# Kernel tuning notes

Hardware: AMD Instinct MI355X
Metric: run time of the kernel (lower is better)

## Reference

```python
import jax, jax.numpy as jnp
import numpy as np

PRIOR_VAR = 0.01
NUM_HEADS = 12
EMBED_DIM = 768


def kl_regularizer(mu, logvar):
    kl_loss = (jnp.log(PRIOR_VAR) - 1.0 - logvar
               + jax.nn.softplus(logvar) / PRIOR_VAR
               + jnp.square(mu) / PRIOR_VAR)
    return 0.5 * jnp.mean(kl_loss)


def linear_vdp(mu_in, Sigma_in, w_mu, w_sigma):
    # mu_in, Sigma_in: [..., Din]; w_mu: [Din, Dout]; w_sigma: [Dout]
    mu_out = mu_in @ w_mu
    kl = kl_regularizer(w_mu, w_sigma)
    W_Sigma = jax.nn.softplus(w_sigma)                      # [Dout]
    din = w_mu.shape[0]
    # w_t_Sigma_i_w: w scaled by sqrt(Din)
    w_scaled = w_mu / jnp.sqrt(jnp.float32(din))
    Sigma_1 = Sigma_in @ (w_scaled * w_scaled)              # [..., Dout]
    # x_Sigma_w_x_T: x scaled by Din
    x = mu_in / jnp.float32(din)
    xx_t = jnp.sum(x * x, axis=-1, keepdims=True)
    Sigma_2 = xx_t * W_Sigma
    # tr_Sigma_w_Sigma_in
    Sigma_3 = jnp.sum(Sigma_in, axis=-1, keepdims=True) * W_Sigma / jnp.float32(w_mu.shape[-1])
    Sigma_out = jax.nn.softplus(Sigma_1 + Sigma_2 + Sigma_3)
    return mu_out, Sigma_out, kl


def split_heads(x, B, H, d):
    # [B, S, E] -> [B, H, S, d]
    return x.reshape(B, -1, H, d).transpose(0, 2, 1, 3)


def vdp_attention(mu_q, sg_q, mu_k, sg_k, mu_v, sg_v):
    d = jnp.float32(mu_k.shape[-1])
    sq = jnp.sqrt(d)
    mu_score = jnp.einsum('bhqd,bhkd->bhqk', mu_q, mu_k)
    a = jnp.einsum('bhqd,bhkd->bhqk', mu_q * mu_q / d, sg_k)
    b = jnp.einsum('bhid,bhjd->bhij', mu_k * mu_k / d, sg_q)  # TF matmul(key.., query.., transpose_b)
    c = jnp.einsum('bhqd,bhkd->bhqk', sg_q / sq, sg_k / sq)
    sigma_score = a + b + c
    mu_weights = jax.nn.softmax(mu_score / sq, axis=-1)
    wdim = jnp.float32(mu_weights.shape[-1])
    grad = jnp.square(mu_weights - mu_weights * mu_weights)
    Sigma_weights = grad * (sigma_score / d) / wdim
    mu_out = jnp.einsum('bhqk,bhkd->bhqd', mu_weights, mu_v)
    dterm = jnp.einsum('bhqk,bhkd->bhqd', mu_weights * mu_weights / wdim, sg_v)
    eterm = jnp.einsum('bhqk,bhkd->bhqd', Sigma_weights, mu_v * mu_v / wdim)
    fterm = jnp.einsum('bhqk,bhkd->bhqd', Sigma_weights / jnp.sqrt(wdim), sg_v / jnp.sqrt(wdim))
    out_sigma = jax.nn.softplus(dterm + eterm + fterm)
    return mu_out, out_sigma


def forward(mu_inputs, sigma_inputs, wq_mu, wq_sigma, wk_mu, wk_sigma,
            wv_mu, wv_sigma, wo_mu, wo_sigma):
    B = mu_inputs.shape[0]
    H = NUM_HEADS
    d = EMBED_DIM // H
    # VDP_Dropout with Training=False is identity
    mu_q, sg_q, kl_q = linear_vdp(mu_inputs, sigma_inputs, wq_mu, wq_sigma)
    mu_k, sg_k, kl_k = linear_vdp(mu_inputs, sigma_inputs, wk_mu, wk_sigma)
    mu_v, sg_v, kl_v = linear_vdp(mu_inputs, sigma_inputs, wv_mu, wv_sigma)
    mu_q, sg_q = split_heads(mu_q, B, H, d), split_heads(sg_q, B, H, d)
    mu_k, sg_k = split_heads(mu_k, B, H, d), split_heads(sg_k, B, H, d)
    mu_v, sg_v = split_heads(mu_v, B, H, d), split_heads(sg_v, B, H, d)
    mu_att, sg_att = vdp_attention(mu_q, sg_q, mu_k, sg_k, mu_v, sg_v)
    mu_cat = mu_att.transpose(0, 2, 1, 3).reshape(B, -1, EMBED_DIM)
    sg_cat = sg_att.transpose(0, 2, 1, 3).reshape(B, -1, EMBED_DIM)
    mu_out, Sigma_out, kl_c = linear_vdp(mu_cat, sg_cat, wo_mu, wo_sigma)
    Sigma_out = jax.nn.softplus(Sigma_out)
    kl = kl_q + kl_k + kl_v + kl_c
    return mu_out, Sigma_out, kl


def setup_inputs() -> dict:
    key = jax.random.key(0)
    ks = jax.random.split(key, 12)
    B, S, E = 4, 1024, EMBED_DIM
    glorot_std = np.sqrt(2.0 / (E + E)).astype(np.float32)
    def wsig(k):
        return jax.random.uniform(k, (E,), jnp.float32, -4.6, -2.25)
    return {
        'mu_inputs': jax.random.normal(ks[0], (B, S, E), jnp.float32),
        'sigma_inputs': jax.random.uniform(ks[1], (B, S, E), jnp.float32),
        'wq_mu': jax.random.normal(ks[2], (E, E), jnp.float32) * glorot_std,
        'wq_sigma': wsig(ks[3]),
        'wk_mu': jax.random.normal(ks[4], (E, E), jnp.float32) * glorot_std,
        'wk_sigma': wsig(ks[5]),
        'wv_mu': jax.random.normal(ks[6], (E, E), jnp.float32) * glorot_std,
        'wv_sigma': wsig(ks[7]),
        'wo_mu': jax.random.normal(ks[8], (E, E), jnp.float32) * glorot_std,
        'wo_sigma': wsig(ks[9]),
    }


def reference(mu_inputs, sigma_inputs, wq_mu, wq_sigma, wk_mu, wk_sigma,
              wv_mu, wv_sigma, wo_mu, wo_sigma):
    return forward(mu_inputs, sigma_inputs, wq_mu, wq_sigma, wk_mu, wk_sigma,
                   wv_mu, wv_sigma, wo_mu, wo_sigma)
```

## Files before the change

### kernel.cpp

```cpp
#include <hip/hip_runtime.h>
#include <math.h>

#define E 768
#define NTOK 4096

typedef __attribute__((ext_vector_type(8))) __bf16 bf16x8;
typedef __attribute__((ext_vector_type(4))) float f32x4;
typedef unsigned int u32;
typedef unsigned short u16;
typedef __attribute__((ext_vector_type(4))) u32 u32x4;

#define BFN ((size_t)NTOK * E)
#define WFN ((size_t)E * E)
#define QSC 1.4901161193847656e-08f
#define C2E 0.18033688011112042f

__device__ __forceinline__ float sp_f(float x) {
    return fmaxf(x, 0.f) + log1pf(__expf(-fabsf(x)));
}
__device__ __forceinline__ u16 f2bf(float f) {
    u32 u = __float_as_uint(f);
    u += 0x7fffu + ((u >> 16) & 1u);
    return (u16)(u >> 16);
}
__device__ __forceinline__ u32 pk2(float a, float b) {
    return (u32)f2bf(a) | ((u32)f2bf(b) << 16);
}
__device__ __forceinline__ u32 cvtpk(float a, float b) {
    u32 r; asm("v_cvt_pk_bf16_f32 %0, %1, %2" : "=v"(r) : "v"(a), "v"(b)); return r;
}
__device__ __forceinline__ float ex2(float x) {
    float r; asm("v_exp_f32 %0, %1" : "=v"(r) : "v"(x)); return r;
}
__device__ __forceinline__ float lg2(float x) {
    float r; asm("v_log_f32 %0, %1" : "=v"(r) : "v"(x)); return r;
}
__device__ __forceinline__ float bfl(u32 u) { return __uint_as_float(u << 16); }
__device__ __forceinline__ float bfh(u32 u) { return __uint_as_float(u & 0xffff0000u); }

#define GLL16(gp, lp) __builtin_amdgcn_global_load_lds( \
    (const __attribute__((address_space(1))) u32*)(gp), \
    (__attribute__((address_space(3))) u32*)(lp), 16, 0, 0)

#define SBAR() do { __builtin_amdgcn_sched_barrier(0); \
                    __builtin_amdgcn_s_barrier(); \
                    __builtin_amdgcn_sched_barrier(0); } while (0)
#define VMCNT(N) do { asm volatile("s_waitcnt vmcnt(" #N ")" ::: "memory"); \
                      __builtin_amdgcn_sched_barrier(0); } while (0)

__global__ __launch_bounds__(256) void prep_all(
    const float* __restrict__ mu_in, const float* __restrict__ sg_in,
    const float* __restrict__ wq, const float* __restrict__ wk,
    const float* __restrict__ wvp, const float* __restrict__ wo,
    const float* __restrict__ wqs, const float* __restrict__ wks,
    const float* __restrict__ wvs, const float* __restrict__ wos,
    u16* __restrict__ Xmu, u16* __restrict__ Xsg,
    float* __restrict__ rmu2, float* __restrict__ rsg,
    u16* __restrict__ WtAll, u16* __restrict__ W2tAll,
    float* __restrict__ spws, float* __restrict__ kl_out)
{
    __shared__ float T[32][33];
    __shared__ float r1[4], r2[4];
    const int b = blockIdx.x, tid = threadIdx.x;

    if (b < 2048) {
        const int half = tid >> 7;
        const int n = b * 2 + half;
        const int t2 = tid & 127;
        float s1 = 0.f, s2 = 0.f;
        if (t2 < 96) {
            size_t o = (size_t)n * E + t2 * 8;
            float4 a0 = *(const float4*)(mu_in + o), a1 = *(const float4*)(mu_in + o + 4);
            float4 b0 = *(const float4*)(sg_in + o), b1 = *(const float4*)(sg_in + o + 4);
            *(uint4*)(Xmu + o) = make_uint4(pk2(a0.x, a0.y), pk2(a0.z, a0.w), pk2(a1.x, a1.y), pk2(a1.z, a1.w));
            *(uint4*)(Xsg + o) = make_uint4(pk2(b0.x, b0.y), pk2(b0.z, b0.w), pk2(b1.x, b1.y), pk2(b1.z, b1.w));
            s1 = a0.x*a0.x + a0.y*a0.y + a0.z*a0.z + a0.w*a0.w + a1.x*a1.x + a1.y*a1.y + a1.z*a1.z + a1.w*a1.w;
            s2 = b0.x + b0.y + b0.z + b0.w + b1.x + b1.y + b1.z + b1.w;
        }
        for (int off = 32; off; off >>= 1) {
            s1 += __shfl_xor(s1, off);
            s2 += __shfl_xor(s2, off);
        }
        if ((tid & 63) == 0) { r1[tid >> 6] = s1; r2[tid >> 6] = s2; }
        __syncthreads();
        if (t2 == 0) {
            rmu2[n] = r1[half * 2] + r1[half * 2 + 1];
            rsg[n]  = r2[half * 2] + r2[half * 2 + 1];
        }
    } else if (b < 4352) {
        const int b2 = b - 2048;
        const int z = b2 / 576, rem = b2 - z * 576;
        const float* W = (z == 0) ? wq : (z == 1) ? wk : (z == 2) ? wvp : wo;
        u16* Wt  = WtAll  + (size_t)z * WFN;
        u16* W2t = W2tAll + (size_t)z * WFN;
        const int j0 = (rem % 24) * 32, k0 = (rem / 24) * 32;
        const int r = tid >> 3, c = (tid & 7) * 4;
        float4 v = *(const float4*)(W + (size_t)(k0 + r) * E + j0 + c);
        T[r][c] = v.x; T[r][c + 1] = v.y; T[r][c + 2] = v.z; T[r][c + 3] = v.w;
        __syncthreads();
        const int j = tid >> 3, kc = (tid & 7) * 4;
        float w0 = T[kc][j], w1 = T[kc + 1][j], w2 = T[kc + 2][j], w3 = T[kc + 3][j];
        size_t o = (size_t)(j0 + j) * E + k0 + kc;
        *(uint2*)(Wt + o) = make_uint2(pk2(w0, w1), pk2(w2, w3));
        const float s = 1.f / 768.f;
        *(uint2*)(W2t + o) = make_uint2(pk2(w0 * w0 * s, w1 * w1 * s), pk2(w2 * w2 * s, w3 * w3 * s));
    } else if (b < 4864) {
        const int gid = (b - 4352) * 256 + tid;
        const int gsz = 512 * 256;
        float acc = 0.f;
        const float cw = 100.f / ((float)E * (float)E);
#pragma unroll
        for (int mm = 0; mm < 4; ++mm) {
            const float* w  = (mm == 0) ? wq  : (mm == 1) ? wk  : (mm == 2) ? wvp : wo;
            const float* sv = (mm == 0) ? wqs : (mm == 1) ? wks : (mm == 2) ? wvs : wos;
            for (int i = gid; i < E * E; i += gsz) { float x = w[i]; acc += x * x * cw; }
            for (int i = gid; i < E; i += gsz) { float x = sv[i]; acc += (-x + sp_f(x) * 100.f) * (1.f / (float)E); }
        }
        if (b == 4352 && tid == 0) acc += 4.f * (logf(0.01f) - 1.f);
        for (int off = 32; off; off >>= 1) acc += __shfl_xor(acc, off);
        if ((tid & 63) == 0) r1[tid >> 6] = acc;
        __syncthreads();
        if (tid == 0) atomicAdd(kl_out, 0.5f * (r1[0] + r1[1] + r1[2] + r1[3]));
    } else {
        for (int i = tid; i < 4 * E; i += 256) {
            const float* src;
            int j;
            if (i < E)            { src = wqs; j = i; }
            else if (i < 2 * E)   { src = wks; j = i - E; }
            else if (i < 3 * E)   { src = wvs; j = i - 2 * E; }
            else                  { src = wos; j = i - 3 * E; }
            spws[i] = sp_f(src[j]);
        }
    }
}

template<int MODE, int NBUF>
__global__ __launch_bounds__(256, 3) void linear_fused(
    const u16* __restrict__ Am, const u16* __restrict__ As,
    const u16* __restrict__ Wt, const u16* __restrict__ W2t,
    const float* __restrict__ spws, const float* __restrict__ rmu2, const float* __restrict__ rsg,
    float* __restrict__ mu_out, float* __restrict__ sg_out, u16* __restrict__ QKVB)
{
    __shared__ __align__(16) u16 L[NBUF * 12288];

    const int wgid = blockIdx.x;
    const int xcd = wgid & 7, local = wgid >> 3;
    const int m_blk = xcd * 4 + (local & 3);
    const int n_blk = local >> 2;
    const int m0 = m_blk * 128, col0 = n_blk * 64;
    const int tid = threadIdx.x, wv = tid >> 6, lane = tid & 63;
    const int g = lane >> 4, q15 = lane & 15;

    const u16* sp_[6];
    {
        const int rA = tid >> 2, cA = tid & 3;
        const int rB = 64 + rA;
        const int csA = (cA ^ ((rA >> 1) & 3)) << 3;
        const int csB = (cA ^ ((rB >> 1) & 3)) << 3;
        sp_[0] = Am  + (size_t)(m0 + rA) * E + csA;
        sp_[1] = Am  + (size_t)(m0 + rB) * E + csB;
        sp_[2] = As  + (size_t)(m0 + rA) * E + csA;
        sp_[3] = As  + (size_t)(m0 + rB) * E + csB;
        sp_[4] = Wt  + (size_t)(col0 + rA) * E + csA;
        sp_[5] = W2t + (size_t)(col0 + rA) * E + csA;
    }

    f32x4 acc1[2][4], acc2[2][4];
#pragma unroll
    for (int mt = 0; mt < 2; ++mt)
#pragma unroll
        for (int nt = 0; nt < 4; ++nt) {
            acc1[mt][nt] = (f32x4){0.f, 0.f, 0.f, 0.f};
            acc2[mt][nt] = (f32x4){0.f, 0.f, 0.f, 0.f};
        }

#pragma unroll
    for (int j = 0; j < 6; ++j)
        GLL16(sp_[j], &L[j * 2048 + tid * 8]);

    for (int t = 0; t < 24; ++t) {
        SBAR();
        const int tn = (t < 23) ? t + 1 : 23;
        const int nb = ((t & 1) ^ 1) * 12288;
#pragma unroll
        for (int j = 0; j < 6; ++j)
            GLL16(sp_[j] + tn * 32, &L[nb + j * 2048 + tid * 8]);
        VMCNT(6);
        SBAR();
        const int cb = (t & 1) * 12288;
        bf16x8 am[2], asg[2];
#pragma unroll
        for (int mt = 0; mt < 2; ++mt) {
            int r = wv * 32 + mt * 16 + q15;
            int c = (g ^ ((r >> 1) & 3)) << 3;
            am[mt]  = *(const bf16x8*)&L[cb + r * 32 + c];
            asg[mt] = *(const bf16x8*)&L[cb + 4096 + r * 32 + c];
        }
        __builtin_amdgcn_s_setprio(1);
#pragma unroll
        for (int nt = 0; nt < 4; ++nt) {
            int rb = nt * 16 + q15;
            int c = (g ^ ((rb >> 1) & 3)) << 3;
            bf16x8 bw = *(const bf16x8*)&L[cb + 8192 + rb * 32 + c];
            bf16x8 b2 = *(const bf16x8*)&L[cb + 10240 + rb * 32 + c];
            acc1[0][nt] = __builtin_amdgcn_mfma_f32_16x16x32_bf16(am[0], bw, acc1[0][nt], 0, 0, 0);
            acc1[1][nt] = __builtin_amdgcn_mfma_f32_16x16x32_bf16(am[1], bw, acc1[1][nt], 0, 0, 0);
            acc2[0][nt] = __builtin_amdgcn_mfma_f32_16x16x32_bf16(asg[0], b2, acc2[0][nt], 0, 0, 0);
            acc2[1][nt] = __builtin_amdgcn_mfma_f32_16x16x32_bf16(asg[1], b2, acc2[1][nt], 0, 0, 0);
        }
        __builtin_amdgcn_s_setprio(0);
    }
    __syncthreads();

    const float inv2 = 1.f / (768.f * 768.f), invd = 1.f / 768.f;
    float rr[2][4];
#pragma unroll
    for (int mt = 0; mt < 2; ++mt)
#pragma unroll
        for (int r = 0; r < 4; ++r) {
            int row = m0 + wv * 32 + mt * 16 + g * 4 + r;
            rr[mt][r] = rmu2[row] * inv2 + rsg[row] * invd;
        }

    if (MODE == 0) {
#pragma unroll
        for (int mt = 0; mt < 2; ++mt)
#pragma unroll
            for (int nt = 0; nt < 4; ++nt)
#pragma unroll
                for (int r = 0; r < 4; ++r) {
                    int row = m0 + wv * 32 + mt * 16 + g * 4 + r;
                    int col = col0 + nt * 16 + q15;
                    float mu = acc1[mt][nt][r];
                    float sg = sp_f(sp_f(acc2[mt][nt][r] + rr[mt][r] * spws[col]));
                    mu_out[(size_t)row * E + col] = mu;
                    sg_out[(size_t)row * E + col] = sg;
                }
    } else {
        const int proj = n_blk / 12, h = n_blk % 12;
        float sgv[2][4][4];
#pragma unroll
        for (int mt = 0; mt < 2; ++mt)
#pragma unroll
            for (int nt = 0; nt < 4; ++nt)
#pragma unroll
                for (int r = 0; r < 4; ++r) {
                    int col = col0 + nt * 16 + q15;
                    sgv[mt][nt][r] = sp_f(acc2[mt][nt][r] + rr[mt][r] * spws[col]);
                }
        const int bb = m0 >> 10;
        if (proj < 2) {
            const int s0 = (m0 & 1023);
            const int sl = tid >> 1, hh = tid & 1;
            size_t gbase = ((size_t)(bb * 12 + h) << 16) + ((size_t)(s0 + sl) << 6) + hh * 32;
#pragma unroll
            for (int a = 0; a < 3; ++a) {
                __syncthreads();
#pragma unroll
                for (int mt = 0; mt < 2; ++mt)
#pragma unroll
                    for (int nt = 0; nt < 4; ++nt)
#pragma unroll
                        for (int r = 0; r < 4; ++r) {
                            float mu = acc1[mt][nt][r], sg = sgv[mt][nt][r];
                            float v = (a == 0) ? mu : (a == 1) ? sg :
                                      (proj == 0 ? (mu * mu + sg) * QSC : mu * mu * QSC);
                            L[(wv * 32 + mt * 16 + g * 4 + r) * 72 + nt * 16 + q15] = f2bf(v);
                        }
                __syncthreads();
                u16* dst = QKVB + (size_t)(proj * 3 + a) * BFN;
#pragma unroll
                for (int j = 0; j < 4; ++j)
                    *(uint4*)(dst + gbase + j * 8) = *(const uint4*)&L[sl * 72 + hh * 32 + j * 8];
            }
        } else {
            const int s0 = m0 & 1023;
#pragma unroll
            for (int a = 0; a < 3; ++a) {
                __syncthreads();
#pragma unroll
                for (int mt = 0; mt < 2; ++mt)
#pragma unroll
                    for (int nt = 0; nt < 4; ++nt)
#pragma unroll
                        for (int r = 0; r < 4; ++r) {
                            float mu = acc1[mt][nt][r], sg = sgv[mt][nt][r];
                            float v = (a == 0) ? mu : (a == 1) ? sg * 0.0009765625f : mu * mu + sg;
                            L[(nt * 16 + q15) * 136 + wv * 32 + g * 8 + mt * 4 + r] = f2bf(v);
                        }
                __syncthreads();
                const int d = tid >> 2, sc = (tid & 3) * 32;
                u16* dst = QKVB + (size_t)(6 + a) * BFN;
                size_t ga = ((size_t)((bb * 12 + h) * 64 + d) << 10) + s0 + sc;
                *(uint4*)(dst + ga)      = *(const uint4*)&L[d * 136 + sc];
                *(uint4*)(dst + ga + 8)  = *(const uint4*)&L[d * 136 + sc + 8];
                *(uint4*)(dst + ga + 16) = *(const uint4*)&L[d * 136 + sc + 16];
                *(uint4*)(dst + ga + 24) = *(const uint4*)&L[d * 136 + sc + 24];
            }
        }
    }
}

#define KB0 0
#define KB1 6144
#define VB0 12288
#define VB1 18432
__global__ __launch_bounds__(256, 3) void vdp_attn9(
    const u16* __restrict__ Kmu, const u16* __restrict__ Ksg, const u16* __restrict__ Asq,
    const u16* __restrict__ Qmu, const u16* __restrict__ Q1v, const u16* __restrict__ Q2v,
    const u16* __restrict__ Vmu, const u16* __restrict__ Vsg, const u16* __restrict__ Vw2,
    u16* __restrict__ om, u16* __restrict__ osg,
    float* __restrict__ armu2, float* __restrict__ arsg)
{
    __shared__ __align__(16) u16 L[24576];

    const int wgid = blockIdx.x;
    const int seq = (wgid & 7) * 96 + (wgid >> 3);
    const int bh = seq >> 4, qt = seq & 15;
    const int tid = threadIdx.x, wv = tid >> 6, lane = tid & 63;
    const int g = lane >> 4, q15 = lane & 15;
    const size_t hb = (size_t)bh << 16;

    const size_t qoff = hb + (size_t)((qt * 64 + wv * 16 + q15) << 6) + g * 8;
    bf16x8 bq0 = *(const bf16x8*)(Qmu + qoff), bq1 = *(const bf16x8*)(Qmu + qoff + 32);
    bf16x8 b10 = *(const bf16x8*)(Q1v + qoff), b11 = *(const bf16x8*)(Q1v + qoff + 32);
    bf16x8 b20 = *(const bf16x8*)(Q2v + qoff), b21 = *(const bf16x8*)(Q2v + qoff + 32);

    const int sr = tid >> 3, sc8 = tid & 7;
    const size_t koffA = hb + (size_t)sr * 64 + ((sc8 ^ (sr & 7)) << 3);
    const int vr = tid >> 2, vc = tid & 3;
    const size_t voff = hb + (size_t)vr * 1024 + ((vc ^ ((vr >> 1) & 3)) << 3);

    float m2 = -3.0e38f;
    float lacc[4] = {0.f, 0.f, 0.f, 0.f};
#pragma unroll
    for (int s = 0; s < 4; ++s)
        GLL16(Kmu + koffA + s * 2048, &L[s * 2048 + tid * 8]);
    __syncthreads();
    for (int t = 0; t < 8; ++t) {
        SBAR();
        const int tn = (t < 7) ? t + 1 : 7;
        const int nb = (t & 1) ? 0 : 8192;
#pragma unroll
        for (int s = 0; s < 4; ++s)
            GLL16(Kmu + koffA + (size_t)tn * 8192 + s * 2048, &L[nb + s * 2048 + tid * 8]);
        VMCNT(4);
        SBAR();
        const int kb = (t & 1) ? 8192 : 0;
        f32x4 sc[8];
#pragma unroll
        for (int kt = 0; kt < 8; ++kt) sc[kt] = (f32x4){0.f, 0.f, 0.f, 0.f};
        __builtin_amdgcn_s_setprio(1);
#pragma unroll
        for (int kt = 0; kt < 8; ++kt) {
            int row = kt * 16 + q15, ra = kb + (row << 6);
            bf16x8 k0 = *(const bf16x8*)&L[ra + ((g ^ (row & 7)) << 3)];
            bf16x8 k1 = *(const bf16x8*)&L[ra + (((g + 4) ^ (row & 7)) << 3)];
            sc[kt] = __builtin_amdgcn_mfma_f32_16x16x32_bf16(k0, bq0, sc[kt], 0, 0, 0);
            sc[kt] = __builtin_amdgcn_mfma_f32_16x16x32_bf16(k1, bq1, sc[kt], 0, 0, 0);
        }
        __builtin_amdgcn_s_setprio(0);
        float tmx = -3.0e38f;
#pragma unroll
        for (int kt = 0; kt < 8; ++kt)
#pragma unroll
            for (int r = 0; r < 4; ++r) tmx = fmaxf(tmx, sc[kt][r]);
        tmx *= C2E;
        if (tmx > m2 + 8.f) {
            float f = ex2(m2 - tmx);
            lacc[0] *= f; lacc[1] *= f; lacc[2] *= f; lacc[3] *= f;
            m2 = tmx;
        }
#pragma unroll
        for (int kt = 0; kt < 8; ++kt)
#pragma unroll
            for (int r = 0; r < 4; ++r)
                lacc[kt & 3] += ex2(fmaf(sc[kt][r], C2E, -m2));
    }
    __syncthreads();
    float l = (lacc[0] + lacc[1]) + (lacc[2] + lacc[3]);
#pragma unroll
    for (int off = 16; off <= 32; off <<= 1) {
        float mo = __shfl_xor(m2, off), lo = __shfl_xor(l, off);
        float nm = fmaxf(m2, mo);
        l = l * ex2(m2 - nm) + lo * ex2(mo - nm);
        m2 = nm;
    }
    const float M = m2 + lg2(l);

    f32x4 accm[4], accd[4], acce[4];
#pragma unroll
    for (int nt = 0; nt < 4; ++nt) {
        accm[nt] = (f32x4){0.f, 0.f, 0.f, 0.f};
        accd[nt] = (f32x4){0.f, 0.f, 0.f, 0.f};
        acce[nt] = (f32x4){0.f, 0.f, 0.f, 0.f};
    }

    GLL16(Kmu + koffA, &L[KB0 + 0    + wv * 512]);
    GLL16(Ksg + koffA, &L[KB0 + 2048 + wv * 512]);
    GLL16(Asq + koffA, &L[KB0 + 4096 + wv * 512]);
    GLL16(Vmu + voff, &L[VB0 + 0    + wv * 512]);
    GLL16(Vsg + voff, &L[VB0 + 2048 + wv * 512]);
    GLL16(Vw2 + voff, &L[VB0 + 4096 + wv * 512]);
    __syncthreads();

    for (int t = 0; t < 32; ++t) {
        SBAR();
        const int tn = (t < 31) ? t + 1 : 31;
        const size_t ka = (size_t)tn << 11;
        const size_t va = (size_t)tn << 5;
        const int nbK = (t & 1) ? KB0 : KB1;
        const int nbV = (t & 1) ? VB0 : VB1;
        GLL16(Kmu + koffA + ka, &L[nbK + 0    + wv * 512]);
        GLL16(Ksg + koffA + ka, &L[nbK + 2048 + wv * 512]);
        GLL16(Asq + koffA + ka, &L[nbK + 4096 + wv * 512]);
        GLL16(Vmu + voff + va,  &L[nbV + 0    + wv * 512]);
        GLL16(Vsg + voff + va,  &L[nbV + 2048 + wv * 512]);
        GLL16(Vw2 + voff + va,  &L[nbV + 4096 + wv * 512]);
        VMCNT(6);
        SBAR();

        const int kb = (t & 1) ? KB1 : KB0;
        const int vb = (t & 1) ? VB1 : VB0;
        f32x4 sc[2], sgc[2];
#pragma unroll
        for (int kt = 0; kt < 2; ++kt) { sc[kt] = (f32x4){0.f,0.f,0.f,0.f}; sgc[kt] = (f32x4){0.f,0.f,0.f,0.f}; }
        __builtin_amdgcn_s_setprio(1);
#pragma unroll
        for (int kt = 0; kt < 2; ++kt) {
            int row = kt * 16 + q15, ra = kb + (row << 6);
            int ca = ((g ^ (row & 7)) << 3), cb = (((g + 4) ^ (row & 7)) << 3);
            sc[kt]  = __builtin_amdgcn_mfma_f32_16x16x32_bf16(*(const bf16x8*)&L[ra + ca],        bq0, sc[kt],  0, 0, 0);
            sc[kt]  = __builtin_amdgcn_mfma_f32_16x16x32_bf16(*(const bf16x8*)&L[ra + cb],        bq1, sc[kt],  0, 0, 0);
            sgc[kt] = __builtin_amdgcn_mfma_f32_16x16x32_bf16(*(const bf16x8*)&L[2048 + ra + ca], b10, sgc[kt], 0, 0, 0);
            sgc[kt] = __builtin_amdgcn_mfma_f32_16x16x32_bf16(*(const bf16x8*)&L[2048 + ra + cb], b11, sgc[kt], 0, 0, 0);
            sgc[kt] = __builtin_amdgcn_mfma_f32_16x16x32_bf16(*(const bf16x8*)&L[4096 + ra + ca], b20, sgc[kt], 0, 0, 0);
            sgc[kt] = __builtin_amdgcn_mfma_f32_16x16x32_bf16(*(const bf16x8*)&L[4096 + ra + cb], b21, sgc[kt], 0, 0, 0);
        }
        __builtin_amdgcn_s_setprio(0);

        float p[8], p2v[8], swv[8];
#pragma unroll
        for (int kt = 0; kt < 2; ++kt)
#pragma unroll
            for (int r = 0; r < 4; ++r) {
                int j = kt * 4 + r;
                float pv = ex2(fmaf(sc[kt][r], C2E, -M));
                float pp = pv * pv;
                float gq = pv - pp;
                p[j] = pv; p2v[j] = pp; swv[j] = gq * gq * sgc[kt][r];
            }
        u32x4 ua  = {cvtpk(p[0], p[1]),     cvtpk(p[2], p[3]),     cvtpk(p[4], p[5]),     cvtpk(p[6], p[7])};
        u32x4 ubv = {cvtpk(p2v[0], p2v[1]), cvtpk(p2v[2], p2v[3]), cvtpk(p2v[4], p2v[5]), cvtpk(p2v[6], p2v[7])};
        u32x4 ucv = {cvtpk(swv[0], swv[1]), cvtpk(swv[2], swv[3]), cvtpk(swv[4], swv[5]), cvtpk(swv[6], swv[7])};
        bf16x8 pa  = *(const bf16x8*)&ua;
        bf16x8 p2a = *(const bf16x8*)&ubv;
        bf16x8 swa = *(const bf16x8*)&ucv;

        __builtin_amdgcn_s_setprio(1);
#pragma unroll
        for (int nt = 0; nt < 4; ++nt) {
            int row = nt * 16 + q15;
            int vi = vb + (row << 5) + ((g ^ ((q15 >> 1) & 3)) << 3);
            accm[nt] = __builtin_amdgcn_mfma_f32_16x16x32_bf16(pa,  *(const bf16x8*)&L[vi],        accm[nt], 0, 0, 0);
            accd[nt] = __builtin_amdgcn_mfma_f32_16x16x32_bf16(p2a, *(const bf16x8*)&L[vi + 2048], accd[nt], 0, 0, 0);
            acce[nt] = __builtin_amdgcn_mfma_f32_16x16x32_bf16(swa, *(const bf16x8*)&L[vi + 4096], acce[nt], 0, 0, 0);
        }
        __builtin_amdgcn_s_setprio(0);
    }

    const int b_ = bh / 12, h_ = bh % 12;
#pragma unroll
    for (int r = 0; r < 4; ++r) {
        int srow = qt * 64 + wv * 16 + g * 4 + r;
        int n = b_ * 1024 + srow;
        float s1 = 0.f, s2 = 0.f;
#pragma unroll
        for (int nt = 0; nt < 4; ++nt) {
            int d = nt * 16 + q15;
            float mu = accm[nt][r];
            float sg = sp_f(accd[nt][r] + acce[nt][r]);
            size_t o = (size_t)n * E + h_ * 64 + d;
            om[o]  = f2bf(mu);
            osg[o] = f2bf(sg);
            s1 += mu * mu;
            s2 += sg;
        }
#pragma unroll
        for (int off = 1; off < 16; off <<= 1) {
            s1 += __shfl_xor(s1, off);
            s2 += __shfl_xor(s2, off);
        }
        if (q15 == 0) {
            atomicAdd(&armu2[n], s1);
            atomicAdd(&arsg[n], s2);
        }
    }
}

extern "C" void kernel_launch(void* const* d_in, const int* in_sizes, int n_in,
                              void* d_out, int out_size, void* d_ws, size_t ws_size,
                              hipStream_t stream)
{
    const float* mu_in = (const float*)d_in[0];
    const float* sg_in = (const float*)d_in[1];
    const float* wq  = (const float*)d_in[2];
    const float* wqs = (const float*)d_in[3];
    const float* wk  = (const float*)d_in[4];
    const float* wks = (const float*)d_in[5];
    const float* wvp = (const float*)d_in[6];
    const float* wvs = (const float*)d_in[7];
    const float* wo  = (const float*)d_in[8];
    const float* wos = (const float*)d_in[9];

    float* out_mu = (float*)d_out;
    float* out_sg = out_mu + (size_t)NTOK * E;
    float* kl_out = out_mu + 2 * (size_t)NTOK * E;

    float* ws = (float*)d_ws;
    size_t off = 0;
    auto allocf = [&](size_t n) { float* p = ws + off; off += n; return p; };
    float* rmu2  = allocf(NTOK);
    float* rsgs  = allocf(NTOK);
    float* armu2 = allocf(NTOK);
    float* arsg  = allocf(NTOK);
    float* spws  = allocf(4 * E);

    u16* ub = (u16*)(ws + off);
    size_t uoff = 0;
    auto allocu = [&](size_t n) { u16* p = ub + uoff; uoff += n; return p; };
    u16* Xmu    = allocu(BFN);
    u16* Xsg    = allocu(BFN);
    u16* WtAll  = allocu(4 * WFN);
    u16* W2tAll = allocu(4 * WFN);
    u16* QKVB   = allocu(9 * BFN);
    u16* amu_b  = allocu(BFN);
    u16* asg_b  = allocu(BFN);
    (void)ws_size; (void)in_sizes; (void)n_in; (void)out_size;

    hipMemsetAsync(kl_out, 0, 4, stream);
    hipMemsetAsync(armu2, 0, 2 * NTOK * sizeof(float), stream);
    prep_all<<<4865, 256, 0, stream>>>(mu_in, sg_in, wq, wk, wvp, wo,
                                       wqs, wks, wvs, wos,
                                       Xmu, Xsg, rmu2, rsgs, WtAll, W2tAll,
                                       spws, kl_out);

    linear_fused<1, 2><<<1152, 256, 0, stream>>>(Xmu, Xsg, WtAll, W2tAll, spws, rmu2, rsgs,
                                                 nullptr, nullptr, QKVB);

    vdp_attn9<<<768, 256, 0, stream>>>(QKVB + 3 * BFN, QKVB + 4 * BFN, QKVB + 1 * BFN,
                                       QKVB + 0 * BFN, QKVB + 2 * BFN, QKVB + 5 * BFN,
                                       QKVB + 6 * BFN, QKVB + 7 * BFN, QKVB + 8 * BFN,
                                       amu_b, asg_b, armu2, arsg);

    linear_fused<0, 2><<<384, 256, 0, stream>>>(amu_b, asg_b, WtAll + 3 * WFN, W2tAll + 3 * WFN,
                                                spws + 3 * E, armu2, arsg,
                                                out_mu, out_sg, nullptr);
}
```

Measured before the change: 222.2 us.

## Fuse KL reduction into weight transpose blocks and retile output projection to 64-row tiles

The KL sum of squared weights is now computed inside the weight-transpose blocks from the values they already load, which removes 512 extra blocks that re-read all four weight matrices. The output projection gets its own kernel with 64x64 tiles and 768 workgroups instead of 128x64 tiles and 384 workgroups, so more blocks are available to fill the CUs. The trade-off is that each workgroup reuses less data, and the transpose blocks now also do a reduction and an atomic add.

After: 234.5 us (median of 2 runs). +5.5%, slower.

```diff
diff --git a/kernel.cpp b/kernel.cpp
--- a/kernel.cpp
+++ b/kernel.cpp
@@ -96,6 +96,16 @@
         const int j0 = (rem % 24) * 32, k0 = (rem / 24) * 32;
         const int r = tid >> 3, c = (tid & 7) * 4;
         float4 v = *(const float4*)(W + (size_t)(k0 + r) * E + j0 + c);
+        const float cw = 100.f / ((float)E * (float)E);
+        float ka = (v.x * v.x + v.y * v.y + v.z * v.z + v.w * v.w) * cw;
+        if (rem == 0) {
+            const float* sv = (z == 0) ? wqs : (z == 1) ? wks : (z == 2) ? wvs : wos;
+            for (int i = tid; i < E; i += 256) {
+                float x = sv[i];
+                ka += (-x + sp_f(x) * 100.f) * (1.f / (float)E);
+            }
+            if (b == 2048 && tid == 0) ka += 4.f * (logf(0.01f) - 1.f);
+        }
         T[r][c] = v.x; T[r][c + 1] = v.y; T[r][c + 2] = v.z; T[r][c + 3] = v.w;
         __syncthreads();
         const int j = tid >> 3, kc = (tid & 7) * 4;
@@ -104,21 +114,8 @@
         *(uint2*)(Wt + o) = make_uint2(pk2(w0, w1), pk2(w2, w3));
         const float s = 1.f / 768.f;
         *(uint2*)(W2t + o) = make_uint2(pk2(w0 * w0 * s, w1 * w1 * s), pk2(w2 * w2 * s, w3 * w3 * s));
-    } else if (b < 4864) {
-        const int gid = (b - 4352) * 256 + tid;
-        const int gsz = 512 * 256;
-        float acc = 0.f;
-        const float cw = 100.f / ((float)E * (float)E);
-#pragma unroll
-        for (int mm = 0; mm < 4; ++mm) {
-            const float* w  = (mm == 0) ? wq  : (mm == 1) ? wk  : (mm == 2) ? wvp : wo;
-            const float* sv = (mm == 0) ? wqs : (mm == 1) ? wks : (mm == 2) ? wvs : wos;
-            for (int i = gid; i < E * E; i += gsz) { float x = w[i]; acc += x * x * cw; }
-            for (int i = gid; i < E; i += gsz) { float x = sv[i]; acc += (-x + sp_f(x) * 100.f) * (1.f / (float)E); }
-        }
-        if (b == 4352 && tid == 0) acc += 4.f * (logf(0.01f) - 1.f);
-        for (int off = 32; off; off >>= 1) acc += __shfl_xor(acc, off);
-        if ((tid & 63) == 0) r1[tid >> 6] = acc;
+        for (int off = 32; off; off >>= 1) ka += __shfl_xor(ka, off);
+        if ((tid & 63) == 0) r1[tid >> 6] = ka;
         __syncthreads();
         if (tid == 0) atomicAdd(kl_out, 0.5f * (r1[0] + r1[1] + r1[2] + r1[3]));
     } else {
@@ -134,14 +131,13 @@
     }
 }
 
-template<int MODE, int NBUF>
-__global__ __launch_bounds__(256, 3) void linear_fused(
+__global__ __launch_bounds__(256, 3) void linear_qkv(
     const u16* __restrict__ Am, const u16* __restrict__ As,
     const u16* __restrict__ Wt, const u16* __restrict__ W2t,
     const float* __restrict__ spws, const float* __restrict__ rmu2, const float* __restrict__ rsg,
-    float* __restrict__ mu_out, float* __restrict__ sg_out, u16* __restrict__ QKVB)
+    u16* __restrict__ QKVB)
 {
-    __shared__ __align__(16) u16 L[NBUF * 12288];
+    __shared__ __align__(16) u16 L[24576];
 
     const int wgid = blockIdx.x;
     const int xcd = wgid & 7, local = wgid >> 3;
@@ -222,81 +218,145 @@
             rr[mt][r] = rmu2[row] * inv2 + rsg[row] * invd;
         }
 
-    if (MODE == 0) {
-#pragma unroll
-        for (int mt = 0; mt < 2; ++mt)
-#pragma unroll
-            for (int nt = 0; nt < 4; ++nt)
-#pragma unroll
-                for (int r = 0; r < 4; ++r) {
-                    int row = m0 + wv * 32 + mt * 16 + g * 4 + r;
-                    int col = col0 + nt * 16 + q15;
-                    float mu = acc1[mt][nt][r];
-                    float sg = sp_f(sp_f(acc2[mt][nt][r] + rr[mt][r] * spws[col]));
-                    mu_out[(size_t)row * E + col] = mu;
-                    sg_out[(size_t)row * E + col] = sg;
-                }
+    const int proj = n_blk / 12, h = n_blk % 12;
+    float sgv[2][4][4];
+#pragma unroll
+    for (int mt = 0; mt < 2; ++mt)
+#pragma unroll
+        for (int nt = 0; nt < 4; ++nt)
+#pragma unroll
+            for (int r = 0; r < 4; ++r) {
+                int col = col0 + nt * 16 + q15;
+                sgv[mt][nt][r] = sp_f(acc2[mt][nt][r] + rr[mt][r] * spws[col]);
+            }
+    const int bb = m0 >> 10;
+    if (proj < 2) {
+        const int s0 = (m0 & 1023);
+        const int sl = tid >> 1, hh = tid & 1;
+        size_t gbase = ((size_t)(bb * 12 + h) << 16) + ((size_t)(s0 + sl) << 6) + hh * 32;
+#pragma unroll
+        for (int a = 0; a < 3; ++a) {
+            __syncthreads();
+#pragma unroll
+            for (int mt = 0; mt < 2; ++mt)
+#pragma unroll
+                for (int nt = 0; nt < 4; ++nt)
+#pragma unroll
+                    for (int r = 0; r < 4; ++r) {
+                        float mu = acc1[mt][nt][r], sg = sgv[mt][nt][r];
+                        float v = (a == 0) ? mu : (a == 1) ? sg :
+                                  (proj == 0 ? (mu * mu + sg) * QSC : mu * mu * QSC);
+                        L[(wv * 32 + mt * 16 + g * 4 + r) * 72 + nt * 16 + q15] = f2bf(v);
+                    }
+            __syncthreads();
+            u16* dst = QKVB + (size_t)(proj * 3 + a) * BFN;
+#pragma unroll
+            for (int j = 0; j < 4; ++j)
+                *(uint4*)(dst + gbase + j * 8) = *(const uint4*)&L[sl * 72 + hh * 32 + j * 8];
+        }
     } else {
-        const int proj = n_blk / 12, h = n_blk % 12;
-        float sgv[2][4][4];
-#pragma unroll
-        for (int mt = 0; mt < 2; ++mt)
-#pragma unroll
-            for (int nt = 0; nt < 4; ++nt)
-#pragma unroll
-                for (int r = 0; r < 4; ++r) {
-                    int col = col0 + nt * 16 + q15;
-                    sgv[mt][nt][r] = sp_f(acc2[mt][nt][r] + rr[mt][r] * spws[col]);
-                }
-        const int bb = m0 >> 10;
-        if (proj < 2) {
-            const int s0 = (m0 & 1023);
-            const int sl = tid >> 1, hh = tid & 1;
-            size_t gbase = ((size_t)(bb * 12 + h) << 16) + ((size_t)(s0 + sl) << 6) + hh * 32;
-#pragma unroll
-            for (int a = 0; a < 3; ++a) {
-                __syncthreads();
-#pragma unroll
-                for (int mt = 0; mt < 2; ++mt)
-#pragma unroll
-                    for (int nt = 0; nt < 4; ++nt)
-#pragma unroll
-                        for (int r = 0; r < 4; ++r) {
-                            float mu = acc1[mt][nt][r], sg = sgv[mt][nt][r];
-                            float v = (a == 0) ? mu : (a == 1) ? sg :
-                                      (proj == 0 ? (mu * mu + sg) * QSC : mu * mu * QSC);
-                            L[(wv * 32 + mt * 16 + g * 4 + r) * 72 + nt * 16 + q15] = f2bf(v);
-                        }
-                __syncthreads();
-                u16* dst = QKVB + (size_t)(proj * 3 + a) * BFN;
-#pragma unroll
-                for (int j = 0; j < 4; ++j)
-                    *(uint4*)(dst + gbase + j * 8) = *(const uint4*)&L[sl * 72 + hh * 32 + j * 8];
-            }
-        } else {
-            const int s0 = m0 & 1023;
-#pragma unroll
-            for (int a = 0; a < 3; ++a) {
-                __syncthreads();
-#pragma unroll
-                for (int mt = 0; mt < 2; ++mt)
-#pragma unroll
-                    for (int nt = 0; nt < 4; ++nt)
-#pragma unroll
-                        for (int r = 0; r < 4; ++r) {
-                            float mu = acc1[mt][nt][r], sg = sgv[mt][nt][r];
-                            float v = (a == 0) ? mu : (a == 1) ? sg * 0.0009765625f : mu * mu + sg;
-                            L[(nt * 16 + q15) * 136 + wv * 32 + g * 8 + mt * 4 + r] = f2bf(v);
-                        }
-                __syncthreads();
-                const int d = tid >> 2, sc = (tid & 3) * 32;
-                u16* dst = QKVB + (size_t)(6 + a) * BFN;
-                size_t ga = ((size_t)((bb * 12 + h) * 64 + d) << 10) + s0 + sc;
-                *(uint4*)(dst + ga)      = *(const uint4*)&L[d * 136 + sc];
-                *(uint4*)(dst + ga + 8)  = *(const uint4*)&L[d * 136 + sc + 8];
-                *(uint4*)(dst + ga + 16) = *(const uint4*)&L[d * 136 + sc + 16];
-                *(uint4*)(dst + ga + 24) = *(const uint4*)&L[d * 136 + sc + 24];
-            }
+        const int s0 = m0 & 1023;
+#pragma unroll
+        for (int a = 0; a < 3; ++a) {
+            __syncthreads();
+#pragma unroll
+            for (int mt = 0; mt < 2; ++mt)
+#pragma unroll
+                for (int nt = 0; nt < 4; ++nt)
+#pragma unroll
+                    for (int r = 0; r < 4; ++r) {
+                        float mu = acc1[mt][nt][r], sg = sgv[mt][nt][r];
+                        float v = (a == 0) ? mu : (a == 1) ? sg * 0.0009765625f : mu * mu + sg;
+                        L[(nt * 16 + q15) * 136 + wv * 32 + g * 8 + mt * 4 + r] = f2bf(v);
+                    }
+            __syncthreads();
+            const int d = tid >> 2, sc = (tid & 3) * 32;
+            u16* dst = QKVB + (size_t)(6 + a) * BFN;
+            size_t ga = ((size_t)((bb * 12 + h) * 64 + d) << 10) + s0 + sc;
+            *(uint4*)(dst + ga)      = *(const uint4*)&L[d * 136 + sc];
+            *(uint4*)(dst + ga + 8)  = *(const uint4*)&L[d * 136 + sc + 8];
+            *(uint4*)(dst + ga + 16) = *(const uint4*)&L[d * 136 + sc + 16];
+            *(uint4*)(dst + ga + 24) = *(const uint4*)&L[d * 136 + sc + 24];
+        }
+    }
+}
+
+__global__ __launch_bounds__(256, 3) void linear_oproj64(
+    const u16* __restrict__ Am, const u16* __restrict__ As,
+    const u16* __restrict__ Wt, const u16* __restrict__ W2t,
+    const float* __restrict__ spws, const float* __restrict__ rmu2, const float* __restrict__ rsg,
+    float* __restrict__ mu_out, float* __restrict__ sg_out)
+{
+    __shared__ __align__(16) u16 L[16384];
+
+    const int wgid = blockIdx.x;
+    const int xcd = wgid & 7, local = wgid >> 3;
+    const int m_blk = xcd * 8 + (local & 7);
+    const int n_blk = local >> 3;
+    const int m0 = m_blk * 64, col0 = n_blk * 64;
+    const int tid = threadIdx.x, wv = tid >> 6, lane = tid & 63;
+    const int g = lane >> 4, q15 = lane & 15;
+
+    const u16* sp_[4];
+    {
+        const int r = tid >> 2, c = tid & 3;
+        const int cs = (c ^ ((r >> 1) & 3)) << 3;
+        sp_[0] = Am  + (size_t)(m0 + r) * E + cs;
+        sp_[1] = As  + (size_t)(m0 + r) * E + cs;
+        sp_[2] = Wt  + (size_t)(col0 + r) * E + cs;
+        sp_[3] = W2t + (size_t)(col0 + r) * E + cs;
+    }
+
+    f32x4 acc1[4], acc2[4];
+#pragma unroll
+    for (int nt = 0; nt < 4; ++nt) {
+        acc1[nt] = (f32x4){0.f, 0.f, 0.f, 0.f};
+        acc2[nt] = (f32x4){0.f, 0.f, 0.f, 0.f};
+    }
+
+#pragma unroll
+    for (int j = 0; j < 4; ++j)
+        GLL16(sp_[j], &L[j * 2048 + tid * 8]);
+
+    for (int t = 0; t < 24; ++t) {
+        SBAR();
+        const int tn = (t < 23) ? t + 1 : 23;
+        const int nb = ((t & 1) ^ 1) * 8192;
+#pragma unroll
+        for (int j = 0; j < 4; ++j)
+            GLL16(sp_[j] + tn * 32, &L[nb + j * 2048 + tid * 8]);
+        VMCNT(4);
+        SBAR();
+        const int cb = (t & 1) * 8192;
+        int rA = wv * 16 + q15;
+        int cA = (g ^ ((rA >> 1) & 3)) << 3;
+        bf16x8 am  = *(const bf16x8*)&L[cb + rA * 32 + cA];
+        bf16x8 asg = *(const bf16x8*)&L[cb + 2048 + rA * 32 + cA];
+        __builtin_amdgcn_s_setprio(1);
+#pragma unroll
+        for (int nt = 0; nt < 4; ++nt) {
+            int rb = nt * 16 + q15;
+            int c = (g ^ ((rb >> 1) & 3)) << 3;
+            bf16x8 bw = *(const bf16x8*)&L[cb + 4096 + rb * 32 + c];
+            bf16x8 b2 = *(const bf16x8*)&L[cb + 6144 + rb * 32 + c];
+            acc1[nt] = __builtin_amdgcn_mfma_f32_16x16x32_bf16(am,  bw, acc1[nt], 0, 0, 0);
+            acc2[nt] = __builtin_amdgcn_mfma_f32_16x16x32_bf16(asg, b2, acc2[nt], 0, 0, 0);
+        }
+        __builtin_amdgcn_s_setprio(0);
+    }
+
+    const float inv2 = 1.f / (768.f * 768.f), invd = 1.f / 768.f;
+#pragma unroll
+    for (int r = 0; r < 4; ++r) {
+        int row = m0 + wv * 16 + g * 4 + r;
+        float rr = rmu2[row] * inv2 + rsg[row] * invd;
+#pragma unroll
+        for (int nt = 0; nt < 4; ++nt) {
+            int col = col0 + nt * 16 + q15;
+            float mu = acc1[nt][r];
+            float sg = sp_f(sp_f(acc2[nt][r] + rr * spws[col]));
+            mu_out[(size_t)row * E + col] = mu;
+            sg_out[(size_t)row * E + col] = sg;
         }
     }
 }
@@ -540,20 +600,18 @@
 
     hipMemsetAsync(kl_out, 0, 4, stream);
     hipMemsetAsync(armu2, 0, 2 * NTOK * sizeof(float), stream);
-    prep_all<<<4865, 256, 0, stream>>>(mu_in, sg_in, wq, wk, wvp, wo,
+    prep_all<<<4353, 256, 0, stream>>>(mu_in, sg_in, wq, wk, wvp, wo,
                                        wqs, wks, wvs, wos,
                                        Xmu, Xsg, rmu2, rsgs, WtAll, W2tAll,
                                        spws, kl_out);
 
-    linear_fused<1, 2><<<1152, 256, 0, stream>>>(Xmu, Xsg, WtAll, W2tAll, spws, rmu2, rsgs,
-                                                 nullptr, nullptr, QKVB);
+    linear_qkv<<<1152, 256, 0, stream>>>(Xmu, Xsg, WtAll, W2tAll, spws, rmu2, rsgs, QKVB);
 
     vdp_attn9<<<768, 256, 0, stream>>>(QKVB + 3 * BFN, QKVB + 4 * BFN, QKVB + 1 * BFN,
                                        QKVB + 0 * BFN, QKVB + 2 * BFN, QKVB + 5 * BFN,
                                        QKVB + 6 * BFN, QKVB + 7 * BFN, QKVB + 8 * BFN,
                                        amu_b, asg_b, armu2, arsg);
 
-    linear_fused<0, 2><<<384, 256, 0, stream>>>(amu_b, asg_b, WtAll + 3 * WFN, W2tAll + 3 * WFN,
-                                                spws + 3 * E, armu2, arsg,
-                                                out_mu, out_sg, nullptr);
-}
+    linear_oproj64<<<768, 256, 0, stream>>>(amu_b, asg_b, WtAll + 3 * WFN, W2tAll + 3 * WFN,
+                                            spws + 3 * E, armu2, arsg, out_mu, out_sg);
+}
```
